# Optimization experiments

Measured on AMD Instinct MI355X. Metric: run time of the kernel, lower is better.

The kernel has to match this reference:

```python
import jax, jax.numpy as jnp
import numpy as np

B, N_TOKENS, D, K = 16, 4096, 256, 4096
COMMITMENT_COST = 0.25


def setup_inputs() -> dict:
    key = jax.random.key(0)
    k1, k2 = jax.random.split(key)
    x = jax.random.normal(k1, (B, N_TOKENS, D), dtype=jnp.float32)
    # nn.Embedding init uniform(-1/K, 1/K); scale is irrelevant to correctness,
    # use the same distribution for fidelity.
    codebook = jax.random.uniform(k2, (K, D), dtype=jnp.float32,
                                  minval=-1.0 / K, maxval=1.0 / K)
    return {"x": x, "codebook": codebook}


def reference(x, codebook):
    Bb, Nn, Dd = x.shape
    x_flat = x.reshape(-1, Dd)                                    # [BN, D]
    dist_sq = (jnp.sum(x_flat * x_flat, axis=1, keepdims=True)
               + jnp.sum(codebook * codebook, axis=1)
               - 2.0 * x_flat @ codebook.T)                       # [BN, K]
    dist_sq = jnp.maximum(dist_sq, 0.0)
    idx = jnp.argmin(dist_sq, axis=1)                             # [BN]
    q_flat = codebook[idx]                                        # [BN, D]
    q = q_flat.reshape(x.shape)

    x_sg = jax.lax.stop_gradient(x_flat)
    q_sg = jax.lax.stop_gradient(q_flat)
    codebook_loss = jnp.mean((q_flat - x_sg) ** 2, axis=-1).reshape(Bb, Nn)
    commit_loss = jnp.mean((x_flat - q_sg) ** 2, axis=-1).reshape(Bb, Nn)
    per_token_loss = codebook_loss + COMMITMENT_COST * commit_loss
    mean_vq_loss = jnp.mean(per_token_loss)

    q_st = x + jax.lax.stop_gradient(q - x)                       # straight-through

    counts = jnp.zeros((codebook.shape[0],), dtype=jnp.float32).at[idx].add(1.0)
    avg_probs = counts / x_flat.shape[0]
    perplexity = jnp.exp(-jnp.sum(avg_probs * jnp.log(avg_probs + 1e-10)))

    return q_st, mean_vq_loss, perplexity, idx
```

## Files before the change

kernel.cpp:

```cpp
#include <hip/hip_runtime.h>
#include <hip/hip_bf16.h>
#include <cstdint>
#include <cstddef>

#define D 256
#define NTOK 65536
#define KCODES 4096
#define Q_ELEMS (NTOK * D)
#define DELTA 3.0e-4f
#define CAP 24

typedef short bf16x8 __attribute__((ext_vector_type(8)));
typedef float f32x4 __attribute__((ext_vector_type(4)));
typedef unsigned short ushort8 __attribute__((ext_vector_type(8)));

__device__ __forceinline__ void gload_lds16(const float* g, float* l) {
  __builtin_amdgcn_global_load_lds(
      (const __attribute__((address_space(1))) void*)(g),
      (__attribute__((address_space(3))) void*)(l), 16, 0, 0);
}
__device__ __forceinline__ unsigned short f2bf(float f) {
  __hip_bfloat16 h = __float2bfloat16(f);
  unsigned short u;
  __builtin_memcpy(&u, &h, 2);
  return u;
}
__device__ __forceinline__ float bf2f(unsigned short u) {
  __hip_bfloat16 h;
  __builtin_memcpy(&h, &u, 2);
  return __bfloat162float(h);
}

__global__ __launch_bounds__(256) void ee_kernel(const float* __restrict__ cb,
                                                 float* __restrict__ se) {
  const int row = blockIdx.x * 4 + (threadIdx.x >> 6);
  const int lane = threadIdx.x & 63;
  const float4 v = reinterpret_cast<const float4*>(cb + (size_t)row * D)[lane];
  double s = (double)v.x * v.x + (double)v.y * v.y +
             (double)v.z * v.z + (double)v.w * v.w;
#pragma unroll
  for (int o = 32; o > 0; o >>= 1) s += __shfl_down(s, o, 64);
  if (lane == 0) se[row] = (float)s;
}

__global__ __launch_bounds__(256) void xx_kernel(const float* __restrict__ x,
                                                 float* __restrict__ sx) {
  const int row = blockIdx.x * 4 + (threadIdx.x >> 6);
  const int lane = threadIdx.x & 63;
  const float4 v = reinterpret_cast<const float4*>(x + (size_t)row * D)[lane];
  double s = (double)v.x * v.x + (double)v.y * v.y +
             (double)v.z * v.z + (double)v.w * v.w;
#pragma unroll
  for (int o = 32; o > 0; o >>= 1) s += __shfl_down(s, o, 64);
  if (lane == 0) sx[row] = (float)s;
}

__global__ __launch_bounds__(256) void pack_e_kernel(const float* __restrict__ cb,
                                                     unsigned short* __restrict__ bpack) {
  const int gid = blockIdx.x * 256 + threadIdx.x;
  const int c = gid >> 2;
  const int kt = gid & 3;
  const int row = c & 127;
  const int swz = (row & 7) << 3;
  unsigned short* dst = bpack + ((size_t)((c >> 7) * 4 + kt)) * 8192 + row * 64;
  const float* src = cb + (size_t)c * D + kt * 64;
#pragma unroll
  for (int j = 0; j < 8; ++j) {
    ushort8 o;
#pragma unroll
    for (int e = 0; e < 8; ++e) o[e] = f2bf(src[j * 8 + e]);
    *reinterpret_cast<ushort8*>(dst + ((j * 8) ^ swz)) = o;
  }
}

__global__ __launch_bounds__(256, 2) void screen3_kernel(
    const float* __restrict__ x, const unsigned short* __restrict__ bpack,
    const float* __restrict__ se, unsigned int* __restrict__ ccnt_g,
    unsigned int* __restrict__ cand_g, float* __restrict__ rm_g) {
  __shared__ __attribute__((aligned(16))) unsigned short bbuf[3][8192];
  __shared__ __attribute__((aligned(16))) unsigned short se_lds[KCODES];
  __shared__ unsigned int cand[128][CAP];
  __shared__ unsigned int ccnt[128];

  const int tid = threadIdx.x;
  const int lane = tid & 63;
  const int w = tid >> 6;
  const int l15 = lane & 15;
  const int kg = lane >> 4;
  const int tok0 = blockIdx.x * 128;

  if (tid < 128) ccnt[tid] = 0;
  {
    const float4* s4 = reinterpret_cast<const float4*>(se) + tid * 4;
    const float4 a = s4[0], b = s4[1], c = s4[2], d = s4[3];
    ushort8 o0, o1;
    o0[0] = f2bf(a.x); o0[1] = f2bf(a.y); o0[2] = f2bf(a.z); o0[3] = f2bf(a.w);
    o0[4] = f2bf(b.x); o0[5] = f2bf(b.y); o0[6] = f2bf(b.z); o0[7] = f2bf(b.w);
    o1[0] = f2bf(c.x); o1[1] = f2bf(c.y); o1[2] = f2bf(c.z); o1[3] = f2bf(c.w);
    o1[4] = f2bf(d.x); o1[5] = f2bf(d.y); o1[6] = f2bf(d.z); o1[7] = f2bf(d.w);
    *reinterpret_cast<ushort8*>(&se_lds[tid * 16]) = o0;
    *reinterpret_cast<ushort8*>(&se_lds[tid * 16 + 8]) = o1;
  }

  bf16x8 ah[2][8];
#pragma unroll
  for (int gi = 0; gi < 2; ++gi) {
    const int t = tok0 + w * 32 + gi * 16 + l15;
    const float* xp = x + (size_t)t * D;
#pragma unroll
    for (int ks = 0; ks < 8; ++ks) {
      const float4 v0 = *reinterpret_cast<const float4*>(xp + ks * 32 + kg * 8);
      const float4 v1 = *reinterpret_cast<const float4*>(xp + ks * 32 + kg * 8 + 4);
      const float xv[8] = {v0.x, v0.y, v0.z, v0.w, v1.x, v1.y, v1.z, v1.w};
      bf16x8 h;
#pragma unroll
      for (int e = 0; e < 8; ++e) h[e] = (short)f2bf(xv[e]);
      ah[gi][ks] = h;
    }
  }

  auto STAGE = [&](int u) {
    const char* s = (const char*)bpack + (size_t)u * 16384 + w * 4096 + lane * 16;
    char* d = (char*)&bbuf[u % 3][0] + w * 4096;
    gload_lds16((const float*)s, (float*)d);
    gload_lds16((const float*)(s + 1024), (float*)(d + 1024));
    gload_lds16((const float*)(s + 2048), (float*)(d + 2048));
    gload_lds16((const float*)(s + 3072), (float*)(d + 3072));
  };

  float rm[2][4];
#pragma unroll
  for (int fr = 0; fr < 2; ++fr)
#pragma unroll
    for (int q = 0; q < 4; ++q) rm[fr][q] = 3.4e38f;

  f32x4 acc[2][8];

  STAGE(0);
  STAGE(1);
  __syncthreads();

  for (int ct4 = 0; ct4 < 32; ++ct4) {
#pragma unroll
    for (int kt = 0; kt < 4; ++kt) {
      const int u = ct4 * 4 + kt;
      if (u + 2 < 128) STAGE(u + 2);
      if (kt == 0) {
#pragma unroll
        for (int fr = 0; fr < 2; ++fr)
#pragma unroll
          for (int fc = 0; fc < 8; ++fc) acc[fr][fc] = (f32x4){0.f, 0.f, 0.f, 0.f};
      }
      const unsigned short* bb = &bbuf[u % 3][0];
#pragma unroll
      for (int kh = 0; kh < 2; ++kh) {
        const int ks = kt * 2 + kh;
        bf16x8 bfrag[8];
#pragma unroll
        for (int fc = 0; fc < 8; ++fc) {
          const int row = fc * 16 + l15;
          const int off = row * 64 + ((kh * 32 + kg * 8) ^ ((row & 7) << 3));
          bfrag[fc] = *reinterpret_cast<const bf16x8*>(bb + off);
        }
#pragma unroll
        for (int fr = 0; fr < 2; ++fr)
#pragma unroll
          for (int fc = 0; fc < 8; ++fc)
            acc[fr][fc] = __builtin_amdgcn_mfma_f32_16x16x32_bf16(
                ah[fr][ks], bfrag[fc], acc[fr][fc], 0, 0, 0);
      }
      if (kt == 3) {
        float sef[8];
#pragma unroll
        for (int fc = 0; fc < 8; ++fc)
          sef[fc] = bf2f(se_lds[ct4 * 128 + fc * 16 + l15]);
#pragma unroll
        for (int fr = 0; fr < 2; ++fr)
#pragma unroll
          for (int q = 0; q < 4; ++q) {
            float m = fmaf(-2.0f, acc[fr][0][q], sef[0]);
#pragma unroll
            for (int fc = 1; fc < 8; ++fc)
              m = fminf(m, fmaf(-2.0f, acc[fr][fc][q], sef[fc]));
            m = fminf(m, __shfl_xor(m, 1, 64));
            m = fminf(m, __shfl_xor(m, 2, 64));
            m = fminf(m, __shfl_xor(m, 4, 64));
            m = fminf(m, __shfl_xor(m, 8, 64));
            rm[fr][q] = fminf(rm[fr][q], m);
            const float thr = rm[fr][q] + DELTA;
            const int tl = w * 32 + fr * 16 + kg * 4 + q;
#pragma unroll
            for (int fc = 0; fc < 8; ++fc) {
              const float s = fmaf(-2.0f, acc[fr][fc][q], sef[fc]);
              if (s <= thr) {
                const unsigned p = atomicAdd(&ccnt[tl], 1u);
                if (p < CAP)
                  cand[tl][p] = ((unsigned)f2bf(s) << 16) |
                                (unsigned)(ct4 * 128 + fc * 16 + l15);
              }
            }
          }
      }
      __syncthreads();
    }
  }

  if (tid < 128) ccnt_g[tok0 + tid] = ccnt[tid];
  if (l15 == 0) {
#pragma unroll
    for (int fr = 0; fr < 2; ++fr)
#pragma unroll
      for (int q = 0; q < 4; ++q)
        rm_g[tok0 + w * 32 + fr * 16 + kg * 4 + q] = rm[fr][q];
  }
  for (int j = tid; j < 128 * CAP; j += 256)
    cand_g[(size_t)tok0 * CAP + j] = cand[j / CAP][j % CAP];
}

__global__ __launch_bounds__(256) void rescore_kernel(
    const float* __restrict__ x, const float* __restrict__ cb,
    const float* __restrict__ se, const unsigned int* __restrict__ ccnt_g,
    const unsigned int* __restrict__ cand_g, const float* __restrict__ rm_g,
    int* __restrict__ idx_i, float* __restrict__ idxf_out,
    unsigned int* __restrict__ ovf_count, int* __restrict__ ovf_list) {
  const int t = blockIdx.x * 256 + threadIdx.x;
  const unsigned n = ccnt_g[t];
  if (n > CAP) {
    const unsigned p = atomicAdd(ovf_count, 1u);
    ovf_list[p] = t;
    return;
  }
  const float thr = rm_g[t] + DELTA;
  int surv = 0;
  int only_c = 0x7fffffff;
  for (unsigned k = 0; k < n; ++k) {
    const unsigned pk = cand_g[(size_t)t * CAP + k];
    if (bf2f((unsigned short)(pk >> 16)) <= thr) {
      ++surv;
      only_c = (int)(pk & 0xFFFFu);
    }
  }
  int bc;
  if (surv == 1) {
    bc = only_c;
  } else {
    const float4* xp = reinterpret_cast<const float4*>(x + (size_t)t * D);
    double sxd = 0.0;
    for (int d4 = 0; d4 < 64; ++d4) {
      const float4 v = xp[d4];
      sxd += (double)v.x * v.x + (double)v.y * v.y +
             (double)v.z * v.z + (double)v.w * v.w;
    }
    const float sxv = (float)sxd;
    float bq = 3.4e38f;
    bc = 0x7fffffff;
    for (unsigned k = 0; k < n; ++k) {
      const unsigned pk = cand_g[(size_t)t * CAP + k];
      if (bf2f((unsigned short)(pk >> 16)) > thr) continue;
      const int c = (int)(pk & 0xFFFFu);
      const float4* cp = reinterpret_cast<const float4*>(cb + (size_t)c * D);
      float acc = 0.0f;
#pragma unroll 8
      for (int d4 = 0; d4 < 64; ++d4) {
        const float4 xv = xp[d4];
        const float4 ev = cp[d4];
        acc = fmaf(xv.x, ev.x, acc);
        acc = fmaf(xv.y, ev.y, acc);
        acc = fmaf(xv.z, ev.z, acc);
        acc = fmaf(xv.w, ev.w, acc);
      }
      const float r = sxv + se[c];
      const float q = r - 2.0f * acc;
      if (q < bq || (q == bq && c < bc)) { bq = q; bc = c; }
    }
  }
  idx_i[t] = bc;
  idxf_out[t] = (float)bc;
}

__global__ __launch_bounds__(256) void ovf_kernel(
    const float* __restrict__ x, const float* __restrict__ cb,
    const float* __restrict__ se, const unsigned int* __restrict__ ovf_count,
    const int* __restrict__ ovf_list, int* __restrict__ idx_i,
    float* __restrict__ idxf_out) {
  __shared__ float bvv[256];
  __shared__ int bii[256];
  __shared__ double shd[256];
  const int tid = threadIdx.x;
  const unsigned cnt = *ovf_count;
  for (unsigned i = blockIdx.x; i < cnt; i += gridDim.x) {
    const int t = ovf_list[i];
    const float xv1 = x[(size_t)t * D + tid];
    shd[tid] = (double)xv1 * xv1;
    __syncthreads();
    for (int o = 128; o > 0; o >>= 1) {
      if (tid < o) shd[tid] += shd[tid + o];
      __syncthreads();
    }
    const float sxv = (float)shd[0];
    __syncthreads();
    const float4* xp = reinterpret_cast<const float4*>(x + (size_t)t * D);
    float bq = 3.4e38f;
    int bc = 0x7fffffff;
    for (int c = tid; c < KCODES; c += 256) {
      const float4* cp = reinterpret_cast<const float4*>(cb + (size_t)c * D);
      float acc = 0.0f;
#pragma unroll 8
      for (int d4 = 0; d4 < 64; ++d4) {
        const float4 xv = xp[d4];
        const float4 ev = cp[d4];
        acc = fmaf(xv.x, ev.x, acc);
        acc = fmaf(xv.y, ev.y, acc);
        acc = fmaf(xv.z, ev.z, acc);
        acc = fmaf(xv.w, ev.w, acc);
      }
      const float r = sxv + se[c];
      const float q = r - 2.0f * acc;
      if (q < bq || (q == bq && c < bc)) { bq = q; bc = c; }
    }
    bvv[tid] = bq;
    bii[tid] = bc;
    __syncthreads();
    for (int o = 128; o > 0; o >>= 1) {
      if (tid < o) {
        const float v2 = bvv[tid + o];
        const int c2 = bii[tid + o];
        if (v2 < bvv[tid] || (v2 == bvv[tid] && c2 < bii[tid])) {
          bvv[tid] = v2;
          bii[tid] = c2;
        }
      }
      __syncthreads();
    }
    if (tid == 0) {
      idx_i[t] = bii[0];
      idxf_out[t] = (float)bii[0];
    }
    __syncthreads();
  }
}

__global__ __launch_bounds__(256) void argmin_fb_kernel(const float* __restrict__ x,
                                                        const float* __restrict__ cb,
                                                        const float* __restrict__ se,
                                                        const float* __restrict__ sx,
                                                        int* __restrict__ idx_out,
                                                        float* __restrict__ idxf_out) {
  __shared__ __attribute__((aligned(16))) float xs[64 * 128];
  __shared__ __attribute__((aligned(16))) float es[64 * 128];
  const int tid = threadIdx.x;
  const int lane = tid & 63;
  const int w = tid >> 6;
  const int wt = w & 1;
  const int wc = w >> 1;
  const int tgl = lane & 7;
  const int cgl = lane >> 3;
  const int t0 = wt * 64 + tgl * 8;
  const int c0 = wc * 64 + cgl * 8;
  const int tok0 = blockIdx.x * 128;
  float sxf[8];
#pragma unroll
  for (int i = 0; i < 8; ++i) sxf[i] = sx[tok0 + t0 + i];
  float bv[8];
  int bi[8];
#pragma unroll
  for (int i = 0; i < 8; ++i) { bv[i] = 3.4e38f; bi[i] = 0; }
  for (int ct = 0; ct < KCODES / 128; ++ct) {
    float acc[8][8] = {};
    for (int kt = 0; kt < 4; ++kt) {
      __syncthreads();
      {
        const float* xsrc = x + (size_t)tok0 * D + kt * 64;
        const float* esrc = cb + (size_t)(ct * 128) * D + kt * 64;
#pragma unroll
        for (int p = 0; p < 8; ++p) {
          const int idx = p * 256 + tid;
          const int t = idx >> 4;
          const int c = idx & 15;
          const int colp = (t + 8 * (c >> 1)) & 127;
          const float4 xv = *reinterpret_cast<const float4*>(xsrc + (size_t)t * D + c * 4);
          float* xd = &xs[(c * 4) * 128 + colp];
          xd[0] = xv.x; xd[128] = xv.y; xd[256] = xv.z; xd[384] = xv.w;
          const float4 ev = *reinterpret_cast<const float4*>(esrc + (size_t)t * D + c * 4);
          float* ed = &es[(c * 4) * 128 + colp];
          ed[0] = ev.x; ed[128] = ev.y; ed[256] = ev.z; ed[384] = ev.w;
        }
      }
      __syncthreads();
      for (int kp = 0; kp < 8; ++kp) {
        const float* xb = &xs[(kp * 8) * 128 + ((t0 + 8 * kp) & 127)];
        const float* eb = &es[(kp * 8) * 128 + ((c0 + 8 * kp) & 127)];
#pragma unroll
        for (int k2 = 0; k2 < 8; ++k2) {
          const float4 xv0 = *reinterpret_cast<const float4*>(xb + k2 * 128);
          const float4 xv1 = *reinterpret_cast<const float4*>(xb + k2 * 128 + 4);
          const float4 ev0 = *reinterpret_cast<const float4*>(eb + k2 * 128);
          const float4 ev1 = *reinterpret_cast<const float4*>(eb + k2 * 128 + 4);
          const float xa[8] = {xv0.x, xv0.y, xv0.z, xv0.w, xv1.x, xv1.y, xv1.z, xv1.w};
          const float ea[8] = {ev0.x, ev0.y, ev0.z, ev0.w, ev1.x, ev1.y, ev1.z, ev1.w};
#pragma unroll
          for (int i = 0; i < 8; ++i)
#pragma unroll
            for (int j = 0; j < 8; ++j) acc[i][j] = fmaf(xa[i], ea[j], acc[i][j]);
        }
      }
    }
#pragma unroll
    for (int j = 0; j < 8; ++j) {
      const int cidx = ct * 128 + c0 + j;
      const float sef = se[cidx];
#pragma unroll
      for (int i = 0; i < 8; ++i) {
        const float r = sxf[i] + sef;
        const float s = r - 2.0f * acc[i][j];
        if (s < bv[i]) { bv[i] = s; bi[i] = cidx; }
      }
    }
  }
  __syncthreads();
  float* red_val = xs;
  int* red_idx = reinterpret_cast<int*>(xs + 128 * 17);
  const int g = wc * 8 + cgl;
#pragma unroll
  for (int i = 0; i < 8; ++i) {
    red_val[(t0 + i) * 17 + g] = bv[i];
    red_idx[(t0 + i) * 17 + g] = bi[i];
  }
  __syncthreads();
  if (tid < 128) {
    float v = red_val[tid * 17 + 0];
    int ix = red_idx[tid * 17 + 0];
#pragma unroll
    for (int gg = 1; gg < 16; ++gg) {
      const float vv = red_val[tid * 17 + gg];
      const int ii = red_idx[tid * 17 + gg];
      if (vv < v || (vv == v && ii < ix)) { v = vv; ix = ii; }
    }
    idx_out[tok0 + tid] = ix;
    idxf_out[tok0 + tid] = (float)ix;
  }
}

__global__ __launch_bounds__(256) void finalize_kernel(const float* __restrict__ x,
                                                       const float* __restrict__ cb,
                                                       const int* __restrict__ idx,
                                                       float* __restrict__ q_out,
                                                       unsigned int* __restrict__ counts,
                                                       double* __restrict__ partials) {
  __shared__ double tok_s[16];
  const int tid = threadIdx.x;
  const int lt = tid >> 4;
  const int ld = tid & 15;
  const int t = blockIdx.x * 16 + lt;
  const int id = idx[t];
  const float* xp = x + (size_t)t * D + ld * 16;
  const float* ep = cb + (size_t)id * D + ld * 16;
  float* qp = q_out + (size_t)t * D + ld * 16;
  float s = 0.0f;
#pragma unroll
  for (int c = 0; c < 4; ++c) {
    const float4 xv = reinterpret_cast<const float4*>(xp)[c];
    const float4 ev = reinterpret_cast<const float4*>(ep)[c];
    const float d0 = ev.x - xv.x, d1 = ev.y - xv.y;
    const float d2 = ev.z - xv.z, d3 = ev.w - xv.w;
    s = fmaf(d0, d0, s);
    s = fmaf(d1, d1, s);
    s = fmaf(d2, d2, s);
    s = fmaf(d3, d3, s);
    float4 qv;
    qv.x = xv.x + d0;
    qv.y = xv.y + d1;
    qv.z = xv.z + d2;
    qv.w = xv.w + d3;
    reinterpret_cast<float4*>(qp)[c] = qv;
  }
#pragma unroll
  for (int o = 8; o > 0; o >>= 1) s += __shfl_down(s, o, 16);
  if (ld == 0) {
    atomicAdd(&counts[id], 1u);
    tok_s[lt] = (double)s;
  }
  __syncthreads();
  if (tid == 0) {
    double bs = 0.0;
    for (int i = 0; i < 16; ++i) bs += tok_s[i];
    partials[blockIdx.x] = bs;
  }
}

__global__ __launch_bounds__(256) void final_kernel(const unsigned int* __restrict__ counts,
                                                    const double* __restrict__ partials,
                                                    float* __restrict__ loss_out,
                                                    float* __restrict__ perp_out) {
  __shared__ double sh[256];
  const int tid = threadIdx.x;
  double ls = 0.0;
  for (int i = tid; i < NTOK / 16; i += 256) ls += partials[i];
  sh[tid] = ls;
  __syncthreads();
#pragma unroll
  for (int o = 128; o > 0; o >>= 1) {
    if (tid < o) sh[tid] += sh[tid + o];
    __syncthreads();
  }
  if (tid == 0) *loss_out = (float)(sh[0] * (1.25 / (256.0 * 65536.0)));
  __syncthreads();
  double hs = 0.0;
  for (int i = tid; i < KCODES; i += 256) {
    const float p = (float)counts[i] / 65536.0f;
    hs += (double)(p * logf(p + 1e-10f));
  }
  sh[tid] = hs;
  __syncthreads();
#pragma unroll
  for (int o = 128; o > 0; o >>= 1) {
    if (tid < o) sh[tid] += sh[tid + o];
    __syncthreads();
  }
  if (tid == 0) *perp_out = expf((float)(-sh[0]));
}

extern "C" void kernel_launch(void* const* d_in, const int* in_sizes, int n_in,
                              void* d_out, int out_size, void* d_ws, size_t ws_size,
                              hipStream_t stream) {
  (void)in_sizes; (void)n_in; (void)out_size;
  const float* x = (const float*)d_in[0];
  const float* cb = (const float*)d_in[1];

  float* out = (float*)d_out;
  float* q_out = out;
  float* loss_out = out + (size_t)Q_ELEMS;
  float* perp_out = out + (size_t)Q_ELEMS + 1;
  float* idxf_out = out + (size_t)Q_ELEMS + 2;

  char* ws = (char*)d_ws;
  float* se = (float*)(ws + 0);
  unsigned int* counts = (unsigned int*)(ws + (16 << 10));
  double* partials = (double*)(ws + (32 << 10));
  int* idx_i = (int*)(ws + (128 << 10));
  float* sx = (float*)(ws + (384 << 10));
  unsigned int* ovf_count = (unsigned int*)(ws + (640 << 10));
  int* ovf_list = (int*)(ws + (644 << 10));
  unsigned int* ccnt_g = (unsigned int*)(ws + (1 << 20));
  float* rm_g = (float*)(ws + (3 << 19));
  unsigned int* cand_g = (unsigned int*)(ws + (2 << 20));
  unsigned short* bpack = (unsigned short*)(ws + (12 << 20));

  hipMemsetAsync(counts, 0, KCODES * sizeof(unsigned int), stream);
  hipMemsetAsync(ovf_count, 0, sizeof(unsigned int), stream);
  ee_kernel<<<KCODES / 4, 256, 0, stream>>>(cb, se);

  if (ws_size >= (size_t)20 * 1024 * 1024) {
    pack_e_kernel<<<64, 256, 0, stream>>>(cb, bpack);
    screen3_kernel<<<NTOK / 128, 256, 0, stream>>>(x, bpack, se, ccnt_g, cand_g,
                                                   rm_g);
    rescore_kernel<<<NTOK / 256, 256, 0, stream>>>(x, cb, se, ccnt_g, cand_g,
                                                   rm_g, idx_i, idxf_out,
                                                   ovf_count, ovf_list);
    ovf_kernel<<<64, 256, 0, stream>>>(x, cb, se, ovf_count, ovf_list,
                                       idx_i, idxf_out);
  } else {
    xx_kernel<<<NTOK / 4, 256, 0, stream>>>(x, sx);
    argmin_fb_kernel<<<NTOK / 128, 256, 0, stream>>>(x, cb, se, sx, idx_i, idxf_out);
  }
  finalize_kernel<<<NTOK / 16, 256, 0, stream>>>(x, cb, idx_i, q_out, counts, partials);
  final_kernel<<<1, 256, 0, stream>>>(counts, partials, loss_out, perp_out);
}
```

Measured before the change: 345.9 us.

## Split screening tile 2x2 across waves to halve LDS B-fragment reads

Each wave in the screening kernel now covers 64 tokens by 64 codes instead of 32 tokens by 128 codes. Each wave holds twice as many x fragments in registers and loads half as many codebook fragments from LDS per MFMA batch, which cuts LDS read traffic. Because the code dimension is now split across wave pairs, partial row minima go through shared memory and need an extra __syncthreads every 128-code chunk before thresholding. The larger A-fragment array raises register pressure and could hurt occupancy under the 2-blocks-per-CU launch bound.

```diff
diff --git a/kernel.cpp b/kernel.cpp
--- a/kernel.cpp
+++ b/kernel.cpp
@@ -73,7 +73,7 @@
   }
 }
 
-__global__ __launch_bounds__(256, 2) void screen3_kernel(
+__global__ __launch_bounds__(256, 2) void screen6_kernel(
     const float* __restrict__ x, const unsigned short* __restrict__ bpack,
     const float* __restrict__ se, unsigned int* __restrict__ ccnt_g,
     unsigned int* __restrict__ cand_g, float* __restrict__ rm_g) {
@@ -81,10 +81,13 @@
   __shared__ __attribute__((aligned(16))) unsigned short se_lds[KCODES];
   __shared__ unsigned int cand[128][CAP];
   __shared__ unsigned int ccnt[128];
+  __shared__ float rmx[128][2];
 
   const int tid = threadIdx.x;
   const int lane = tid & 63;
   const int w = tid >> 6;
+  const int th = w & 1;
+  const int ch = w >> 1;
   const int l15 = lane & 15;
   const int kg = lane >> 4;
   const int tok0 = blockIdx.x * 128;
@@ -102,10 +105,10 @@
     *reinterpret_cast<ushort8*>(&se_lds[tid * 16 + 8]) = o1;
   }
 
-  bf16x8 ah[2][8];
-#pragma unroll
-  for (int gi = 0; gi < 2; ++gi) {
-    const int t = tok0 + w * 32 + gi * 16 + l15;
+  bf16x8 ah[4][8];
+#pragma unroll
+  for (int gi = 0; gi < 4; ++gi) {
+    const int t = tok0 + th * 64 + gi * 16 + l15;
     const float* xp = x + (size_t)t * D;
 #pragma unroll
     for (int ks = 0; ks < 8; ++ks) {
@@ -128,13 +131,13 @@
     gload_lds16((const float*)(s + 3072), (float*)(d + 3072));
   };
 
-  float rm[2][4];
-#pragma unroll
-  for (int fr = 0; fr < 2; ++fr)
+  float rm[4][4];
+#pragma unroll
+  for (int fr = 0; fr < 4; ++fr)
 #pragma unroll
     for (int q = 0; q < 4; ++q) rm[fr][q] = 3.4e38f;
 
-  f32x4 acc[2][8];
+  f32x4 acc[4][4];
 
   STAGE(0);
   STAGE(1);
@@ -147,56 +150,64 @@
       if (u + 2 < 128) STAGE(u + 2);
       if (kt == 0) {
 #pragma unroll
-        for (int fr = 0; fr < 2; ++fr)
-#pragma unroll
-          for (int fc = 0; fc < 8; ++fc) acc[fr][fc] = (f32x4){0.f, 0.f, 0.f, 0.f};
+        for (int fr = 0; fr < 4; ++fr)
+#pragma unroll
+          for (int fc = 0; fc < 4; ++fc) acc[fr][fc] = (f32x4){0.f, 0.f, 0.f, 0.f};
       }
       const unsigned short* bb = &bbuf[u % 3][0];
 #pragma unroll
       for (int kh = 0; kh < 2; ++kh) {
         const int ks = kt * 2 + kh;
-        bf16x8 bfrag[8];
-#pragma unroll
-        for (int fc = 0; fc < 8; ++fc) {
-          const int row = fc * 16 + l15;
+        bf16x8 bfrag[4];
+#pragma unroll
+        for (int fc = 0; fc < 4; ++fc) {
+          const int row = ch * 64 + fc * 16 + l15;
           const int off = row * 64 + ((kh * 32 + kg * 8) ^ ((row & 7) << 3));
           bfrag[fc] = *reinterpret_cast<const bf16x8*>(bb + off);
         }
 #pragma unroll
-        for (int fr = 0; fr < 2; ++fr)
-#pragma unroll
-          for (int fc = 0; fc < 8; ++fc)
+        for (int fr = 0; fr < 4; ++fr)
+#pragma unroll
+          for (int fc = 0; fc < 4; ++fc)
             acc[fr][fc] = __builtin_amdgcn_mfma_f32_16x16x32_bf16(
                 ah[fr][ks], bfrag[fc], acc[fr][fc], 0, 0, 0);
       }
       if (kt == 3) {
-        float sef[8];
-#pragma unroll
-        for (int fc = 0; fc < 8; ++fc)
-          sef[fc] = bf2f(se_lds[ct4 * 128 + fc * 16 + l15]);
-#pragma unroll
-        for (int fr = 0; fr < 2; ++fr)
+        float sef[4];
+#pragma unroll
+        for (int fc = 0; fc < 4; ++fc)
+          sef[fc] = bf2f(se_lds[ct4 * 128 + ch * 64 + fc * 16 + l15]);
+#pragma unroll
+        for (int fr = 0; fr < 4; ++fr)
 #pragma unroll
           for (int q = 0; q < 4; ++q) {
             float m = fmaf(-2.0f, acc[fr][0][q], sef[0]);
 #pragma unroll
-            for (int fc = 1; fc < 8; ++fc)
+            for (int fc = 1; fc < 4; ++fc)
               m = fminf(m, fmaf(-2.0f, acc[fr][fc][q], sef[fc]));
             m = fminf(m, __shfl_xor(m, 1, 64));
             m = fminf(m, __shfl_xor(m, 2, 64));
             m = fminf(m, __shfl_xor(m, 4, 64));
             m = fminf(m, __shfl_xor(m, 8, 64));
-            rm[fr][q] = fminf(rm[fr][q], m);
+            if (l15 == 0) rmx[th * 64 + fr * 16 + kg * 4 + q][ch] = m;
+          }
+        __syncthreads();
+#pragma unroll
+        for (int fr = 0; fr < 4; ++fr)
+#pragma unroll
+          for (int q = 0; q < 4; ++q) {
+            const int tl = th * 64 + fr * 16 + kg * 4 + q;
+            const float mg = fminf(rmx[tl][0], rmx[tl][1]);
+            rm[fr][q] = fminf(rm[fr][q], mg);
             const float thr = rm[fr][q] + DELTA;
-            const int tl = w * 32 + fr * 16 + kg * 4 + q;
-#pragma unroll
-            for (int fc = 0; fc < 8; ++fc) {
+#pragma unroll
+            for (int fc = 0; fc < 4; ++fc) {
               const float s = fmaf(-2.0f, acc[fr][fc][q], sef[fc]);
               if (s <= thr) {
                 const unsigned p = atomicAdd(&ccnt[tl], 1u);
                 if (p < CAP)
                   cand[tl][p] = ((unsigned)f2bf(s) << 16) |
-                                (unsigned)(ct4 * 128 + fc * 16 + l15);
+                                (unsigned)(ct4 * 128 + ch * 64 + fc * 16 + l15);
               }
             }
           }
@@ -206,12 +217,12 @@
   }
 
   if (tid < 128) ccnt_g[tok0 + tid] = ccnt[tid];
-  if (l15 == 0) {
-#pragma unroll
-    for (int fr = 0; fr < 2; ++fr)
+  if (ch == 0 && l15 == 0) {
+#pragma unroll
+    for (int fr = 0; fr < 4; ++fr)
 #pragma unroll
       for (int q = 0; q < 4; ++q)
-        rm_g[tok0 + w * 32 + fr * 16 + kg * 4 + q] = rm[fr][q];
+        rm_g[tok0 + th * 64 + fr * 16 + kg * 4 + q] = rm[fr][q];
   }
   for (int j = tid; j < 128 * CAP; j += 256)
     cand_g[(size_t)tok0 * CAP + j] = cand[j / CAP][j % CAP];
@@ -552,7 +563,7 @@
 
   if (ws_size >= (size_t)20 * 1024 * 1024) {
     pack_e_kernel<<<64, 256, 0, stream>>>(cb, bpack);
-    screen3_kernel<<<NTOK / 128, 256, 0, stream>>>(x, bpack, se, ccnt_g, cand_g,
+    screen6_kernel<<<NTOK / 128, 256, 0, stream>>>(x, bpack, se, ccnt_g, cand_g,
                                                    rm_g);
     rescore_kernel<<<NTOK / 256, 256, 0, stream>>>(x, cb, se, ccnt_g, cand_g,
                                                    rm_g, idx_i, idxf_out,
```

New measurement: 415.1 us. 1.2x slower.
